# Kernel optimization log

Measured on AMD Instinct MI355X. Metric: run time of the kernel, lower is better.

The kernel has to match this reference:

```python
import jax, jax.numpy as jnp
import numpy as np

PAD = float(-2**32 + 1)
NUM_HEADS = 16
LN_EPS = 1e-5


def _split_heads(x, h):
    # torch.cat(torch.chunk(x, h, dim=2), dim=0): head-major stacking
    B, T, D = x.shape
    d = D // h
    return x.reshape(B, T, h, d).transpose(2, 0, 1, 3).reshape(h * B, T, d)


def _merge_heads(x, h):
    # torch.cat(torch.chunk(x, h, dim=0), dim=2)
    hB, T, d = x.shape
    B = hB // h
    return x.reshape(h, B, T, d).transpose(1, 2, 0, 3).reshape(B, T, h * d)


def setup_inputs() -> dict:
    key = jax.random.key(0)
    ks = jax.random.split(key, 12)
    B, T, D = 2, 2048, 1024
    s = 1.0 / np.sqrt(D)
    return {
        "q": jax.random.normal(ks[0], (B, T, D), jnp.float32),
        "k": jax.random.normal(ks[1], (B, T, D), jnp.float32),
        "v": jax.random.normal(ks[2], (B, T, D), jnp.float32),
        "mask": jax.random.randint(ks[3], (B, T), 0, 2, jnp.int32),
        "causality": 0,
        "edge_fea": jnp.zeros((1,), jnp.float32),
        "wq": jax.random.normal(ks[4], (D, D), jnp.float32) * s,
        "bq": jax.random.normal(ks[5], (D,), jnp.float32) * 0.01,
        "wk": jax.random.normal(ks[6], (D, D), jnp.float32) * s,
        "bk": jax.random.normal(ks[7], (D,), jnp.float32) * 0.01,
        "wv": jax.random.normal(ks[8], (D, D), jnp.float32) * s,
        "bv": jax.random.normal(ks[9], (D,), jnp.float32) * 0.01,
        "gamma": jnp.ones((D,), jnp.float32),
        "beta": jnp.zeros((D,), jnp.float32),
    }


def reference(q, k, v, mask, causality, edge_fea, wq, bq, wk, bk, wv, bv, gamma, beta):
    h = NUM_HEADS
    B, T, D = q.shape
    depth = D // h

    qh = _split_heads(q @ wq.T + bq, h)   # (h*B, T, depth)
    kh = _split_heads(k @ wk.T + bk, h)
    vh = _split_heads(v @ wv.T + bv, h)

    scores = jnp.einsum('ntd,nsd->nts', qh, kh) / jnp.sqrt(jnp.asarray(depth, qh.dtype))
    # key mask: repeat_interleave over dim 0 (batch-major), 1 => masked
    km = jnp.repeat(mask.astype(scores.dtype), h, axis=0)[:, None, :]  # (h*B,1,T)
    scores = scores + km * PAD
    if causality:
        tril = jnp.tril(jnp.ones((T, T), scores.dtype))
        scores = jnp.where(tril[None] == 0, jnp.full_like(scores, PAD), scores)
    attn = jax.nn.softmax(scores, axis=-1)
    ctx = jnp.einsum('nts,nsd->ntd', attn, vh)

    out = _merge_heads(ctx, h) + q  # dropout is identity in eval mode
    # LayerNorm over last dim
    mu = jnp.mean(out, axis=-1, keepdims=True)
    var = jnp.var(out, axis=-1, keepdims=True)
    out = (out - mu) / jnp.sqrt(var + LN_EPS) * gamma + beta
    return out
```

## Files before the change

### kernel.cpp

```cpp
#include <hip/hip_runtime.h>
#include <hip/hip_bf16.h>
#include <stdint.h>

#define B_ 2
#define T_ 2048
#define D_ 1024
#define H_ 16
#define DEPTH 64

typedef unsigned short u16;
typedef unsigned int u32;
typedef short bf16x8 __attribute__((ext_vector_type(8)));
typedef float f32x4 __attribute__((ext_vector_type(4)));

#define MFMA16(a, b, c) __builtin_amdgcn_mfma_f32_16x16x32_bf16(a, b, c, 0, 0, 0)

#if __has_builtin(__builtin_amdgcn_exp2f)
#define EXP2(x) __builtin_amdgcn_exp2f(x)
#else
#define EXP2(x) __expf((x) * 0.6931471805599453f)
#endif

#define GLOAD_LDS(g, l)                                                      \
    __builtin_amdgcn_global_load_lds(                                        \
        (__attribute__((address_space(1))) void*)(g),                        \
        (__attribute__((address_space(3))) void*)(l), 16, 0, 0)

__device__ __forceinline__ float bf2f(u32 u) {
    union { u32 i; float f; } x; x.i = u << 16; return x.f;
}
__device__ __forceinline__ u16 f2bf(float f) {
    union { float f; u32 i; } x; x.f = f;
    u32 r = x.i + 0x7fffu + ((x.i >> 16) & 1u);
    return (u16)(r >> 16);
}
__device__ __forceinline__ uint2 pk4(float4 f) {
    return make_uint2((u32)f2bf(f.x) | ((u32)f2bf(f.y) << 16),
                      (u32)f2bf(f.z) | ((u32)f2bf(f.w) << 16));
}
__device__ __forceinline__ u32 pkfast(float a, float b) {
    union { float f; u32 i; } x, y; x.f = a; y.f = b;
    return ((y.i + 0x8000u) & 0xffff0000u) | ((x.i + 0x8000u) >> 16);
}

__global__ __launch_bounds__(256) void conv_kernel(
    const float* __restrict__ s0, const float* __restrict__ s1, const float* __restrict__ s2,
    const float* __restrict__ s3, const float* __restrict__ s4, const float* __restrict__ s5,
    u16* __restrict__ xbf, u16* __restrict__ wbf)
{
    const int z = blockIdx.y;
    const float* src = (z == 0) ? s0 : (z == 1) ? s1 : (z == 2) ? s2
                     : (z == 3) ? s3 : (z == 4) ? s4 : s5;
    u16* dst = (z < 3) ? (xbf + (size_t)z * 4194304) : (wbf + (size_t)(z - 3) * 1048576);
    const size_t nel = (z < 3) ? 4194304u : 1048576u;
    for (size_t i = ((size_t)blockIdx.x * 256 + threadIdx.x) * 8; i < nel;
         i += (size_t)gridDim.x * 2048) {
        float4 a = *(const float4*)(src + i);
        float4 b = *(const float4*)(src + i + 4);
        uint2 lo = pk4(a), hi = pk4(b);
        *(uint4*)(dst + i) = make_uint4(lo.x, lo.y, hi.x, hi.y);
    }
}

__global__ __launch_bounds__(256, 3) void proj_mfma(
    const u16* __restrict__ xbf, const u16* __restrict__ wbf,
    const float* __restrict__ bq, const float* __restrict__ bk, const float* __restrict__ bv,
    u16* __restrict__ qh, u16* __restrict__ kh, u16* __restrict__ vt)
{
    __shared__ __attribute__((aligned(16))) u16 As[128 * 64];
    __shared__ __attribute__((aligned(16))) u16 Bs[128 * 64];

    const int z = blockIdx.z;
    const u16* A = xbf + (size_t)z * 4194304;
    const u16* W = wbf + (size_t)z * 1048576;
    const float* bias = (z == 0) ? bq : (z == 1) ? bk : bv;

    const int tid = threadIdx.x, w = tid >> 6, lane = tid & 63;
    const int quad = lane >> 4, l16 = lane & 15;
    const int m0 = blockIdx.y * 128, n0 = blockIdx.x * 128;
    const int wm = (w & 1) * 64, wn = (w >> 1) * 64;
    const int srow = lane >> 3;
    const int schunk = (lane & 7) ^ srow;

    f32x4 acc[4][4];
    #pragma unroll
    for (int mi = 0; mi < 4; ++mi)
        #pragma unroll
        for (int ni = 0; ni < 4; ++ni) acc[mi][ni] = (f32x4){0.f, 0.f, 0.f, 0.f};

    const size_t ar = (size_t)(m0 + 32 * w + srow);
    const size_t br = (size_t)(n0 + 32 * w + srow);

    for (int k0 = 0; k0 < D_; k0 += 64) {
        __syncthreads();
        #pragma unroll
        for (int i = 0; i < 4; ++i) {
            GLOAD_LDS(A + (ar + 8 * i) * D_ + k0 + schunk * 8, &As[(32 * w + 8 * i) * 64]);
            GLOAD_LDS(W + (br + 8 * i) * D_ + k0 + schunk * 8, &Bs[(32 * w + 8 * i) * 64]);
        }
        __syncthreads();

        #pragma unroll
        for (int kg = 0; kg < 2; ++kg) {
            const int ch = ((4 * kg + quad) ^ (l16 & 7)) * 8;
            bf16x8 af[4], bf[4];
            #pragma unroll
            for (int mi = 0; mi < 4; ++mi)
                af[mi] = *(const bf16x8*)&As[(wm + 16 * mi + l16) * 64 + ch];
            #pragma unroll
            for (int ni = 0; ni < 4; ++ni)
                bf[ni] = *(const bf16x8*)&Bs[(wn + 16 * ni + l16) * 64 + ch];
            #pragma unroll
            for (int mi = 0; mi < 4; ++mi)
                #pragma unroll
                for (int ni = 0; ni < 4; ++ni)
                    acc[mi][ni] = MFMA16(af[mi], bf[ni], acc[mi][ni]);
        }
    }

    float bl[4];
    #pragma unroll
    for (int ni = 0; ni < 4; ++ni) bl[ni] = bias[n0 + wn + ni * 16 + l16];

    #pragma unroll
    for (int mi = 0; mi < 4; ++mi) {
        const int mb = m0 + wm + mi * 16 + quad * 4;
        #pragma unroll
        for (int ni = 0; ni < 4; ++ni) {
            const int nn = n0 + wn + ni * 16 + l16;
            const int head = nn >> 6, d = nn & 63;
            if (z < 2) {
                u16* outp = (z == 0) ? qh : kh;
                #pragma unroll
                for (int r = 0; r < 4; ++r) {
                    const int m = mb + r;
                    const int b = m >> 11, t = m & (T_ - 1);
                    outp[((size_t)(head * B_ + b) * T_ + t) * DEPTH + d] =
                        f2bf(acc[mi][ni][r] + bl[ni]);
                }
            } else {
                const int b = mb >> 11, t = mb & (T_ - 1);
                float4 f = make_float4(acc[mi][ni][0] + bl[ni], acc[mi][ni][1] + bl[ni],
                                       acc[mi][ni][2] + bl[ni], acc[mi][ni][3] + bl[ni]);
                *(uint2*)(vt + ((size_t)(head * B_ + b) * DEPTH + d) * T_ + t) = pk4(f);
            }
        }
    }
}

__global__ __launch_bounds__(256, 4) void attn_kernel(
    const u16* __restrict__ qh, const u16* __restrict__ kh, const u16* __restrict__ vt,
    const int* __restrict__ maskp, const int* __restrict__ causp,
    u16* __restrict__ po, float* __restrict__ pl)
{
    __shared__ __attribute__((aligned(16))) u16 Ks[64 * 64];
    __shared__ __attribute__((aligned(16))) u16 Vs[64 * 64];
    __shared__ __attribute__((aligned(16))) u16 Ps[4][2][16][72];
    __shared__ __attribute__((aligned(16))) float padf[1024];

    const int n  = blockIdx.y;
    const int qt = blockIdx.x;
    const int kk = blockIdx.z;
    const int kbase = kk * 1024;
    const int head = n >> 1, bi = n & 1;
    const int mrow = n >> 4;
    const int caus = causp[0];

    const int tid  = threadIdx.x;
    const int w    = tid >> 6, lane = tid & 63;
    const int quad = lane >> 4, l16 = lane & 15;
    const size_t base = (size_t)n * T_ * DEPTH;
    const size_t vbase = (size_t)n * DEPTH * T_;
    const size_t elems = (size_t)B_ * T_ * D_;

    const float C1  = 0.18033688011112042f;
    const float PL2 = -6.2e9f;

    {
        const int i0 = tid * 4;
        int4 m = *(const int4*)(maskp + (size_t)mrow * T_ + kbase + i0);
        padf[i0 + 0] = (float)m.x * PL2; padf[i0 + 1] = (float)m.y * PL2;
        padf[i0 + 2] = (float)m.z * PL2; padf[i0 + 3] = (float)m.w * PL2;
    }

    bf16x8 aq[2][2];
    #pragma unroll
    for (int s = 0; s < 2; ++s) {
        const int qg = qt * 128 + w * 32 + s * 16 + l16;
        aq[s][0] = *(const bf16x8*)(qh + base + (size_t)qg * DEPTH + quad * 8);
        aq[s][1] = *(const bf16x8*)(qh + base + (size_t)qg * DEPTH + 32 + quad * 8);
    }

    f32x4 O[2][4];
    #pragma unroll
    for (int s = 0; s < 2; ++s)
        #pragma unroll
        for (int t = 0; t < 4; ++t) O[s][t] = (f32x4){0.f, 0.f, 0.f, 0.f};
    float lp[2] = {0.f, 0.f};

    const int g_row = w * 16 + (lane >> 3);
    const int g_ch  = (lane & 7) ^ ((lane >> 3) & 7);
    const u16* ksrc = kh + base + (size_t)g_row * DEPTH + g_ch * 8;
    const u16* vsrc = vt + vbase + (size_t)g_row * T_ + g_ch * 8;

    for (int t0 = kbase; t0 < kbase + 1024; t0 += 64) {
        __syncthreads();
        GLOAD_LDS(ksrc + (size_t)t0 * DEPTH,       &Ks[(w * 16) * 64]);
        GLOAD_LDS(ksrc + (size_t)(t0 + 8) * DEPTH, &Ks[(w * 16 + 8) * 64]);
        GLOAD_LDS(vsrc + t0,                       &Vs[(w * 16) * 64]);
        GLOAD_LDS(vsrc + (size_t)8 * T_ + t0,      &Vs[(w * 16 + 8) * 64]);
        __syncthreads();

        const int swz = (l16 & 7);
        const int lt0 = t0 - kbase;
        #pragma unroll
        for (int t = 0; t < 4; ++t) {
            const int krow = t * 16 + l16;
            bf16x8 kb0 = *(const bf16x8*)&Ks[krow * 64 + ((quad ^ swz) * 8)];
            bf16x8 kb1 = *(const bf16x8*)&Ks[krow * 64 + (((4 + quad) ^ swz) * 8)];
            f32x4 pv4 = *(const f32x4*)&padf[lt0 + t * 16 + quad * 4];
            #pragma unroll
            for (int s = 0; s < 2; ++s) {
                f32x4 st = (f32x4){0.f, 0.f, 0.f, 0.f};
                st = MFMA16(kb0, aq[s][0], st);
                st = MFMA16(kb1, aq[s][1], st);
                float v0 = fmaf(st[0], C1, pv4[0]);
                float v1 = fmaf(st[1], C1, pv4[1]);
                float v2 = fmaf(st[2], C1, pv4[2]);
                float v3 = fmaf(st[3], C1, pv4[3]);
                if (caus) {
                    const int kg = t0 + t * 16 + quad * 4;
                    const int qg = qt * 128 + w * 32 + s * 16 + l16;
                    if (kg + 0 > qg) v0 = PL2;
                    if (kg + 1 > qg) v1 = PL2;
                    if (kg + 2 > qg) v2 = PL2;
                    if (kg + 3 > qg) v3 = PL2;
                }
                const float e0 = EXP2(v0), e1 = EXP2(v1);
                const float e2 = EXP2(v2), e3 = EXP2(v3);
                lp[s] += (e0 + e1) + (e2 + e3);
                *(uint2*)&Ps[w][s][l16][t * 16 + quad * 4] =
                    make_uint2(pkfast(e0, e1), pkfast(e2, e3));
            }
        }

        bf16x8 ap[2][2];
        #pragma unroll
        for (int s = 0; s < 2; ++s) {
            ap[s][0] = *(const bf16x8*)&Ps[w][s][l16][quad * 8];
            ap[s][1] = *(const bf16x8*)&Ps[w][s][l16][32 + quad * 8];
        }
        #pragma unroll
        for (int t = 0; t < 4; ++t) {
            const int drow = t * 16 + l16;
            bf16x8 vb0 = *(const bf16x8*)&Vs[drow * 64 + ((quad ^ swz) * 8)];
            bf16x8 vb1 = *(const bf16x8*)&Vs[drow * 64 + (((4 + quad) ^ swz) * 8)];
            #pragma unroll
            for (int s = 0; s < 2; ++s) {
                O[s][t] = MFMA16(ap[s][0], vb0, O[s][t]);
                O[s][t] = MFMA16(ap[s][1], vb1, O[s][t]);
            }
        }
    }

    u16* pop = po + (size_t)kk * elems;
    float* plp = pl + (size_t)kk * 32 * T_;
    #pragma unroll
    for (int s = 0; s < 2; ++s) {
        lp[s] += __shfl_xor(lp[s], 16, 64);
        lp[s] += __shfl_xor(lp[s], 32, 64);
        if (quad == 0)
            plp[(size_t)n * T_ + qt * 128 + w * 32 + s * 16 + l16] = lp[s];
    }

    #pragma unroll
    for (int s = 0; s < 2; ++s) {
        #pragma unroll
        for (int r = 0; r < 4; ++r) {
            const int qg = qt * 128 + w * 32 + s * 16 + quad * 4 + r;
            const size_t rb = ((size_t)bi * T_ + qg) * D_ + head * DEPTH + l16;
            pop[rb + 0]  = f2bf(O[s][0][r]);
            pop[rb + 16] = f2bf(O[s][1][r]);
            pop[rb + 32] = f2bf(O[s][2][r]);
            pop[rb + 48] = f2bf(O[s][3][r]);
        }
    }
}

__global__ __launch_bounds__(256) void fuse_ln(
    const u16* __restrict__ po, const float* __restrict__ pl,
    const float* __restrict__ qin,
    const float* __restrict__ gamma, const float* __restrict__ beta,
    float* __restrict__ out)
{
    const int row = blockIdx.x;
    const int bi = row >> 11, t = row & (T_ - 1);
    const int tid = threadIdx.x;
    const size_t elems = (size_t)B_ * T_ * D_;

    const int head = tid >> 4;
    const size_t li = (size_t)(head * B_ + bi) * T_ + t;
    const float l = pl[li] + pl[32 * T_ + li];
    const float inv = 1.0f / fmaxf(l, 1e-30f);

    const size_t basei = (size_t)row * D_ + (tid << 2);
    uint2 a = *(const uint2*)(po + basei);
    uint2 b = *(const uint2*)(po + elems + basei);
    float4 qv = *(const float4*)(qin + basei);
    float x[4];
    x[0] = (bf2f(a.x & 0xffffu) + bf2f(b.x & 0xffffu)) * inv + qv.x;
    x[1] = (bf2f(a.x >> 16)     + bf2f(b.x >> 16))     * inv + qv.y;
    x[2] = (bf2f(a.y & 0xffffu) + bf2f(b.y & 0xffffu)) * inv + qv.z;
    x[3] = (bf2f(a.y >> 16)     + bf2f(b.y >> 16))     * inv + qv.w;

    float s  = x[0] + x[1] + x[2] + x[3];
    float s2 = x[0]*x[0] + x[1]*x[1] + x[2]*x[2] + x[3]*x[3];
    #pragma unroll
    for (int off = 1; off < 64; off <<= 1) {
        s  += __shfl_xor(s, off, 64);
        s2 += __shfl_xor(s2, off, 64);
    }
    __shared__ float rs[4], rs2[4];
    const int wid = tid >> 6;
    if ((tid & 63) == 0) { rs[wid] = s; rs2[wid] = s2; }
    __syncthreads();
    s  = rs[0] + rs[1] + rs[2] + rs[3];
    s2 = rs2[0] + rs2[1] + rs2[2] + rs2[3];
    const float mean = s * (1.0f / (float)D_);
    const float var  = s2 * (1.0f / (float)D_) - mean * mean;
    const float rstd = rsqrtf(var + 1e-5f);
    float4 g = *(const float4*)(gamma + (tid << 2));
    float4 bb = *(const float4*)(beta + (tid << 2));
    float4 r;
    r.x = (x[0] - mean) * rstd * g.x + bb.x;
    r.y = (x[1] - mean) * rstd * g.y + bb.y;
    r.z = (x[2] - mean) * rstd * g.z + bb.z;
    r.w = (x[3] - mean) * rstd * g.w + bb.w;
    *(float4*)(out + basei) = r;
}

extern "C" void kernel_launch(void* const* d_in, const int* in_sizes, int n_in,
                              void* d_out, int out_size, void* d_ws, size_t ws_size,
                              hipStream_t stream)
{
    (void)in_sizes; (void)n_in; (void)out_size; (void)ws_size;
    const float* q    = (const float*)d_in[0];
    const float* k    = (const float*)d_in[1];
    const float* v    = (const float*)d_in[2];
    const int* mask = (const int*)d_in[3];
    const int* caus = (const int*)d_in[4];
    const float* wq = (const float*)d_in[6];
    const float* bq = (const float*)d_in[7];
    const float* wk = (const float*)d_in[8];
    const float* bk = (const float*)d_in[9];
    const float* wv = (const float*)d_in[10];
    const float* bv = (const float*)d_in[11];
    const float* gamma = (const float*)d_in[12];
    const float* beta  = (const float*)d_in[13];
    float* out = (float*)d_out;

    const size_t elems = (size_t)B_ * T_ * D_;
    u16* qh  = (u16*)d_ws;
    u16* kh  = qh + elems;
    u16* vt  = kh + elems;
    u16* xbf = vt + elems;
    u16* wbf = xbf + 3 * elems;
    u16* po   = xbf;
    float* pl = (float*)(po + 2 * elems);

    conv_kernel<<<dim3(512, 6), 256, 0, stream>>>(q, k, v, wq, wk, wv, xbf, wbf);
    proj_mfma<<<dim3(8, 32, 3), 256, 0, stream>>>(xbf, wbf, bq, bk, bv, qh, kh, vt);

    dim3 agrid(T_ / 128, H_ * B_, 2);
    attn_kernel<<<agrid, 256, 0, stream>>>(qh, kh, vt, mask, caus, po, pl);

    fuse_ln<<<B_ * T_, 256, 0, stream>>>(po, pl, q, gamma, beta, out);
}
```

Before: 219.9 us.

## Switch attention to 32x32 MFMA with register-resident P and double-buffered K/V

Rewrites the attention inner loop to use 32x32x16 bf16 MFMA instead of 16x16x32. The S-tile output layout lets the exponentiated probabilities be packed directly into A-operand registers via v_cvt_pk_bf16_f32, so the LDS round trip for P is gone. K/V tiles are now double-buffered, with the next tile's global-to-LDS load issued before computing on the current one, and one barrier per iteration instead of two. This adds register pressure and split 8-byte V reads from LDS, which could reduce occupancy or cause bank conflicts.

```diff
diff --git a/kernel.cpp b/kernel.cpp
--- a/kernel.cpp
+++ b/kernel.cpp
@@ -11,9 +11,12 @@
 typedef unsigned short u16;
 typedef unsigned int u32;
 typedef short bf16x8 __attribute__((ext_vector_type(8)));
+typedef short bf16x4 __attribute__((ext_vector_type(4)));
 typedef float f32x4 __attribute__((ext_vector_type(4)));
+typedef float f32x16 __attribute__((ext_vector_type(16)));
 
 #define MFMA16(a, b, c) __builtin_amdgcn_mfma_f32_16x16x32_bf16(a, b, c, 0, 0, 0)
+#define MFMA32(a, b, c) __builtin_amdgcn_mfma_f32_32x32x16_bf16(a, b, c, 0, 0, 0)
 
 #if __has_builtin(__builtin_amdgcn_exp2f)
 #define EXP2(x) __builtin_amdgcn_exp2f(x)
@@ -38,9 +41,27 @@
     return make_uint2((u32)f2bf(f.x) | ((u32)f2bf(f.y) << 16),
                       (u32)f2bf(f.z) | ((u32)f2bf(f.w) << 16));
 }
-__device__ __forceinline__ u32 pkfast(float a, float b) {
-    union { float f; u32 i; } x, y; x.f = a; y.f = b;
-    return ((y.i + 0x8000u) & 0xffff0000u) | ((x.i + 0x8000u) >> 16);
+__device__ __forceinline__ u32 cvtpk(float lo, float hi) {
+    u32 r;
+    asm("v_cvt_pk_bf16_f32 %0, %1, %2" : "=v"(r) : "v"(lo), "v"(hi));
+    return r;
+}
+__device__ __forceinline__ bf16x8 pk_frag(u32 a, u32 b, u32 c, u32 d) {
+    union { u32 u[4]; bf16x8 v; } x;
+    x.u[0] = a; x.u[1] = b; x.u[2] = c; x.u[3] = d;
+    return x.v;
+}
+__device__ __forceinline__ bf16x8 cat44(bf16x4 a, bf16x4 b) {
+    bf16x8 r;
+    r[0] = a[0]; r[1] = a[1]; r[2] = a[2]; r[3] = a[3];
+    r[4] = b[0]; r[5] = b[1]; r[6] = b[2]; r[7] = b[3];
+    return r;
+}
+__device__ __forceinline__ f32x16 zero16() {
+    f32x16 z;
+    #pragma unroll
+    for (int i = 0; i < 16; ++i) z[i] = 0.f;
+    return z;
 }
 
 __global__ __launch_bounds__(256) void conv_kernel(
@@ -153,9 +174,8 @@
     const int* __restrict__ maskp, const int* __restrict__ causp,
     u16* __restrict__ po, float* __restrict__ pl)
 {
-    __shared__ __attribute__((aligned(16))) u16 Ks[64 * 64];
-    __shared__ __attribute__((aligned(16))) u16 Vs[64 * 64];
-    __shared__ __attribute__((aligned(16))) u16 Ps[4][2][16][72];
+    __shared__ __attribute__((aligned(16))) u16 Ks[2][64 * 64];
+    __shared__ __attribute__((aligned(16))) u16 Vs[2][64 * 64];
     __shared__ __attribute__((aligned(16))) float padf[1024];
 
     const int n  = blockIdx.y;
@@ -168,8 +188,8 @@
 
     const int tid  = threadIdx.x;
     const int w    = tid >> 6, lane = tid & 63;
-    const int quad = lane >> 4, l16 = lane & 15;
-    const size_t base = (size_t)n * T_ * DEPTH;
+    const int l32  = lane & 31, h = lane >> 5;
+    const size_t base  = (size_t)n * T_ * DEPTH;
     const size_t vbase = (size_t)n * DEPTH * T_;
     const size_t elems = (size_t)B_ * T_ * D_;
 
@@ -183,107 +203,104 @@
         padf[i0 + 2] = (float)m.z * PL2; padf[i0 + 3] = (float)m.w * PL2;
     }
 
-    bf16x8 aq[2][2];
-    #pragma unroll
-    for (int s = 0; s < 2; ++s) {
-        const int qg = qt * 128 + w * 32 + s * 16 + l16;
-        aq[s][0] = *(const bf16x8*)(qh + base + (size_t)qg * DEPTH + quad * 8);
-        aq[s][1] = *(const bf16x8*)(qh + base + (size_t)qg * DEPTH + 32 + quad * 8);
-    }
-
-    f32x4 O[2][4];
-    #pragma unroll
-    for (int s = 0; s < 2; ++s)
-        #pragma unroll
-        for (int t = 0; t < 4; ++t) O[s][t] = (f32x4){0.f, 0.f, 0.f, 0.f};
-    float lp[2] = {0.f, 0.f};
+    const int qg = qt * 128 + w * 32 + l32;
+    bf16x8 aq[4];
+    #pragma unroll
+    for (int c = 0; c < 4; ++c)
+        aq[c] = *(const bf16x8*)(qh + base + (size_t)qg * DEPTH + c * 16 + h * 8);
+
+    f32x16 O0 = zero16(), O1 = zero16();
+    float lp = 0.f;
 
     const int g_row = w * 16 + (lane >> 3);
     const int g_ch  = (lane & 7) ^ ((lane >> 3) & 7);
     const u16* ksrc = kh + base + (size_t)g_row * DEPTH + g_ch * 8;
     const u16* vsrc = vt + vbase + (size_t)g_row * T_ + g_ch * 8;
 
-    for (int t0 = kbase; t0 < kbase + 1024; t0 += 64) {
+#define STAGE(bf_, t0_)                                                           \
+    do {                                                                          \
+        GLOAD_LDS(ksrc + (size_t)(t0_) * DEPTH,       &Ks[bf_][(w * 16) * 64]);   \
+        GLOAD_LDS(ksrc + (size_t)((t0_) + 8) * DEPTH, &Ks[bf_][(w * 16 + 8) * 64]); \
+        GLOAD_LDS(vsrc + (t0_),                       &Vs[bf_][(w * 16) * 64]);   \
+        GLOAD_LDS(vsrc + (size_t)8 * T_ + (t0_),      &Vs[bf_][(w * 16 + 8) * 64]); \
+    } while (0)
+
+    STAGE(0, kbase);
+    __syncthreads();
+
+    for (int it = 0; it < 16; ++it) {
+        const int cur = it & 1;
+        if (it < 15) STAGE(cur ^ 1, kbase + (it + 1) * 64);
+
+        const int lt0 = it * 64;
+        bf16x8 pa[2][2];
+        #pragma unroll
+        for (int kb = 0; kb < 2; ++kb) {
+            const int krow = kb * 32 + l32;
+            const u16* krp = &Ks[cur][krow * 64];
+            const int ksw = krow & 7;
+            f32x16 st = zero16();
+            #pragma unroll
+            for (int c = 0; c < 4; ++c) {
+                bf16x8 kf = *(const bf16x8*)(krp + (((c * 2 + h) ^ ksw) * 8));
+                st = MFMA32(kf, aq[c], st);
+            }
+            u32 pk[8];
+            #pragma unroll
+            for (int g = 0; g < 4; ++g) {
+                f32x4 pv = *(const f32x4*)&padf[lt0 + kb * 32 + g * 8 + h * 4];
+                #pragma unroll
+                for (int m2 = 0; m2 < 2; ++m2) {
+                    const int r0 = g * 4 + m2 * 2;
+                    float v0 = fmaf(st[r0],     C1, pv[m2 * 2]);
+                    float v1 = fmaf(st[r0 + 1], C1, pv[m2 * 2 + 1]);
+                    if (caus) {
+                        const int kg = kbase + lt0 + kb * 32 + g * 8 + h * 4 + m2 * 2;
+                        if (kg     > qg) v0 = PL2;
+                        if (kg + 1 > qg) v1 = PL2;
+                    }
+                    const float e0 = EXP2(v0), e1 = EXP2(v1);
+                    lp += e0 + e1;
+                    pk[g * 2 + m2] = cvtpk(e0, e1);
+                }
+            }
+            pa[kb][0] = pk_frag(pk[0], pk[1], pk[2], pk[3]);
+            pa[kb][1] = pk_frag(pk[4], pk[5], pk[6], pk[7]);
+        }
+
+        #pragma unroll
+        for (int dblk = 0; dblk < 2; ++dblk) {
+            const int d = dblk * 32 + l32;
+            const u16* vrp = &Vs[cur][d * 64 + 4 * h];
+            const int vsw = d & 7;
+            #pragma unroll
+            for (int kb = 0; kb < 2; ++kb)
+                #pragma unroll
+                for (int kc = 0; kc < 2; ++kc) {
+                    const int p0 = (kb * 4 + kc * 2) ^ vsw;
+                    bf16x4 vlo = *(const bf16x4*)(vrp + p0 * 8);
+                    bf16x4 vhi = *(const bf16x4*)(vrp + (p0 ^ 1) * 8);
+                    bf16x8 vf = cat44(vlo, vhi);
+                    if (dblk == 0) O0 = MFMA32(pa[kb][kc], vf, O0);
+                    else           O1 = MFMA32(pa[kb][kc], vf, O1);
+                }
+        }
         __syncthreads();
-        GLOAD_LDS(ksrc + (size_t)t0 * DEPTH,       &Ks[(w * 16) * 64]);
-        GLOAD_LDS(ksrc + (size_t)(t0 + 8) * DEPTH, &Ks[(w * 16 + 8) * 64]);
-        GLOAD_LDS(vsrc + t0,                       &Vs[(w * 16) * 64]);
-        GLOAD_LDS(vsrc + (size_t)8 * T_ + t0,      &Vs[(w * 16 + 8) * 64]);
-        __syncthreads();
-
-        const int swz = (l16 & 7);
-        const int lt0 = t0 - kbase;
-        #pragma unroll
-        for (int t = 0; t < 4; ++t) {
-            const int krow = t * 16 + l16;
-            bf16x8 kb0 = *(const bf16x8*)&Ks[krow * 64 + ((quad ^ swz) * 8)];
-            bf16x8 kb1 = *(const bf16x8*)&Ks[krow * 64 + (((4 + quad) ^ swz) * 8)];
-            f32x4 pv4 = *(const f32x4*)&padf[lt0 + t * 16 + quad * 4];
-            #pragma unroll
-            for (int s = 0; s < 2; ++s) {
-                f32x4 st = (f32x4){0.f, 0.f, 0.f, 0.f};
-                st = MFMA16(kb0, aq[s][0], st);
-                st = MFMA16(kb1, aq[s][1], st);
-                float v0 = fmaf(st[0], C1, pv4[0]);
-                float v1 = fmaf(st[1], C1, pv4[1]);
-                float v2 = fmaf(st[2], C1, pv4[2]);
-                float v3 = fmaf(st[3], C1, pv4[3]);
-                if (caus) {
-                    const int kg = t0 + t * 16 + quad * 4;
-                    const int qg = qt * 128 + w * 32 + s * 16 + l16;
-                    if (kg + 0 > qg) v0 = PL2;
-                    if (kg + 1 > qg) v1 = PL2;
-                    if (kg + 2 > qg) v2 = PL2;
-                    if (kg + 3 > qg) v3 = PL2;
-                }
-                const float e0 = EXP2(v0), e1 = EXP2(v1);
-                const float e2 = EXP2(v2), e3 = EXP2(v3);
-                lp[s] += (e0 + e1) + (e2 + e3);
-                *(uint2*)&Ps[w][s][l16][t * 16 + quad * 4] =
-                    make_uint2(pkfast(e0, e1), pkfast(e2, e3));
-            }
-        }
-
-        bf16x8 ap[2][2];
-        #pragma unroll
-        for (int s = 0; s < 2; ++s) {
-            ap[s][0] = *(const bf16x8*)&Ps[w][s][l16][quad * 8];
-            ap[s][1] = *(const bf16x8*)&Ps[w][s][l16][32 + quad * 8];
-        }
-        #pragma unroll
-        for (int t = 0; t < 4; ++t) {
-            const int drow = t * 16 + l16;
-            bf16x8 vb0 = *(const bf16x8*)&Vs[drow * 64 + ((quad ^ swz) * 8)];
-            bf16x8 vb1 = *(const bf16x8*)&Vs[drow * 64 + (((4 + quad) ^ swz) * 8)];
-            #pragma unroll
-            for (int s = 0; s < 2; ++s) {
-                O[s][t] = MFMA16(ap[s][0], vb0, O[s][t]);
-                O[s][t] = MFMA16(ap[s][1], vb1, O[s][t]);
-            }
-        }
-    }
-
+    }
+#undef STAGE
+
+    lp += __shfl_xor(lp, 32, 64);
     u16* pop = po + (size_t)kk * elems;
     float* plp = pl + (size_t)kk * 32 * T_;
-    #pragma unroll
-    for (int s = 0; s < 2; ++s) {
-        lp[s] += __shfl_xor(lp[s], 16, 64);
-        lp[s] += __shfl_xor(lp[s], 32, 64);
-        if (quad == 0)
-            plp[(size_t)n * T_ + qt * 128 + w * 32 + s * 16 + l16] = lp[s];
-    }
-
-    #pragma unroll
-    for (int s = 0; s < 2; ++s) {
-        #pragma unroll
-        for (int r = 0; r < 4; ++r) {
-            const int qg = qt * 128 + w * 32 + s * 16 + quad * 4 + r;
-            const size_t rb = ((size_t)bi * T_ + qg) * D_ + head * DEPTH + l16;
-            pop[rb + 0]  = f2bf(O[s][0][r]);
-            pop[rb + 16] = f2bf(O[s][1][r]);
-            pop[rb + 32] = f2bf(O[s][2][r]);
-            pop[rb + 48] = f2bf(O[s][3][r]);
-        }
+    if (lane < 32)
+        plp[(size_t)n * T_ + qt * 128 + w * 32 + l32] = lp;
+
+    #pragma unroll
+    for (int r = 0; r < 16; ++r) {
+        const int q = qt * 128 + w * 32 + (r & 3) + 8 * (r >> 2) + 4 * h;
+        const size_t rb = ((size_t)bi * T_ + q) * D_ + head * DEPTH + l32;
+        pop[rb]      = f2bf(O0[r]);
+        pop[rb + 32] = f2bf(O1[r]);
     }
 }
 
```

New measurement: 220.4 us. Within noise of the previous version (+0.2%).
